# Performance work log

Hardware: AMD Instinct MI355X
Metric: run time of the kernel (lower is better)

The kernel has to match this reference:

```python
import jax, jax.numpy as jnp
import numpy as np

N_NODES = 50000
N_EDGES = 25000  # hyperedges
NNZ = 400000     # incidence pairs


def _segment_mean(x, idx, num_segments):
    s = jax.ops.segment_sum(x, idx, num_segments=num_segments)
    cnt = jax.ops.segment_sum(jnp.ones((x.shape[0], 1), x.dtype), idx, num_segments=num_segments)
    return s / jnp.maximum(cnt, 1.0)


def _unigcn_conv(X, W, vertex, edges, degE, degV):
    # X: [N, Cin] -> [N, Cout]
    X = X @ W                                   # linear (no bias)
    Xve = X[vertex]                             # gather per incidence [nnz, C]
    Xe = _segment_mean(Xve, edges, N_EDGES)     # first_aggregate='mean' over hyperedges
    Xe = Xe * degE                              # [M,1] scale
    Xev = Xe[edges]                             # gather back [nnz, C]
    Xv = jax.ops.segment_sum(Xev, vertex, num_segments=N_NODES)
    return Xv * degV                            # [N,1] scale


def setup_inputs() -> dict:
    key = jax.random.key(0)
    ks = jax.random.split(key, 8)
    nfeat, nhid_total, nclass = 512, 512, 40
    def glorot(k, fan_in, fan_out):
        std = np.sqrt(6.0 / (fan_in + fan_out))
        return jax.random.uniform(k, (fan_in, fan_out), jnp.float32, -std, std)
    return {
        "X": jax.random.normal(ks[0], (N_NODES, nfeat), jnp.float32),
        "vertex": jax.random.randint(ks[1], (NNZ,), 0, N_NODES, jnp.int32),
        "edges": jax.random.randint(ks[2], (NNZ,), 0, N_EDGES, jnp.int32),
        "W1": glorot(ks[3], nfeat, nhid_total),
        "W2": glorot(ks[4], nhid_total, nhid_total),
        "Wout": glorot(ks[5], nhid_total, nclass),
        "degE": jax.random.uniform(ks[6], (N_EDGES, 1), jnp.float32, 0.1, 1.0),
        "degV": jax.random.uniform(ks[7], (N_NODES, 1), jnp.float32, 0.1, 1.0),
    }


def reference(X, vertex, edges, W1, W2, Wout, degE, degV):
    # dropout layers are identity at eval (rates = 0)
    X = jax.nn.relu(_unigcn_conv(X, W1, vertex, edges, degE, degV))
    X = jax.nn.relu(_unigcn_conv(X, W2, vertex, edges, degE, degV))
    X = _unigcn_conv(X, Wout, vertex, edges, degE, degV)
    return jax.nn.log_softmax(X, axis=1)
```

## Files before the change

kernel.cpp:

```cpp
#include <hip/hip_runtime.h>

#define N_NODES 50000
#define N_EDGES_C 25000
#define NNZ_C 400000
#define SCHUNK 2048

typedef __bf16 bf16;
typedef __bf16 bf16x8 __attribute__((ext_vector_type(8)));
typedef __bf16 bf16x4 __attribute__((ext_vector_type(4)));
typedef float f32x4 __attribute__((ext_vector_type(4)));

typedef __attribute__((address_space(1))) const void as1_cvoid;
typedef __attribute__((address_space(3))) void as3_void;

__device__ __forceinline__ void gload_lds16(const bf16* g, bf16* l) {
  __builtin_amdgcn_global_load_lds((as1_cvoid*)g, (as3_void*)l, 16, 0, 0);
}

__global__ void hist_kernel(const int* __restrict__ vtx, const int* __restrict__ edg,
                            int* __restrict__ cntV, int* __restrict__ cntE, int nnz) {
  int i = blockIdx.x * blockDim.x + threadIdx.x;
  if (i < nnz) {
    atomicAdd(&cntV[vtx[i]], 1);
    atomicAdd(&cntE[edg[i]], 1);
  }
}

__global__ void scan_part2(const int* __restrict__ cntE, const int* __restrict__ cntV,
                           int* __restrict__ partE, int* __restrict__ partV,
                           int nbE) {
  __shared__ int red[256];
  const int t = threadIdx.x;
  const int isV = (blockIdx.x >= nbE);
  const int b = isV ? (blockIdx.x - nbE) : blockIdx.x;
  const int* cnt = isV ? cntV : cntE;
  const int n = isV ? N_NODES : N_EDGES_C;
  const int base = b * SCHUNK + t * 8;
  int s = 0;
#pragma unroll
  for (int q = 0; q < 8; ++q) {
    int i = base + q;
    if (i < n) s += cnt[i];
  }
  red[t] = s;
  __syncthreads();
  for (int d = 128; d > 0; d >>= 1) {
    if (t < d) red[t] += red[t + d];
    __syncthreads();
  }
  if (t == 0) (isV ? partV : partE)[b] = red[0];
}

__global__ void scan_mid2(int* __restrict__ partE, int* __restrict__ partV,
                          int* __restrict__ eoff, int* __restrict__ voff,
                          int nbE, int nbV) {
  const int wv = threadIdx.x >> 6;
  const int lane = threadIdx.x & 63;
  int* part = wv ? partV : partE;
  int* off = wv ? voff : eoff;
  const int np = wv ? nbV : nbE;
  const int n = wv ? N_NODES : N_EDGES_C;
  int orig = (lane < np) ? part[lane] : 0;
  int v = orig;
  for (int o = 1; o < 64; o <<= 1) {
    int x = __shfl_up(v, o);
    if (lane >= o) v += x;
  }
  if (lane < np) part[lane] = v - orig;
  if (lane == 63) off[n] = v;
}

__global__ void scan_final2(const int* __restrict__ cntE, const int* __restrict__ cntV,
                            const int* __restrict__ partE, const int* __restrict__ partV,
                            int* __restrict__ eoff, int* __restrict__ voff, int nbE) {
  __shared__ int tsum[256];
  const int t = threadIdx.x;
  const int isV = (blockIdx.x >= nbE);
  const int b = isV ? (blockIdx.x - nbE) : blockIdx.x;
  const int* cnt = isV ? cntV : cntE;
  const int* part = isV ? partV : partE;
  int* off = isV ? voff : eoff;
  const int n = isV ? N_NODES : N_EDGES_C;
  const int base = b * SCHUNK + t * 8;
  int loc[8];
  int s = 0;
#pragma unroll
  for (int q = 0; q < 8; ++q) {
    int i = base + q;
    loc[q] = (i < n) ? cnt[i] : 0;
    s += loc[q];
  }
  tsum[t] = s;
  __syncthreads();
  for (int d = 1; d < 256; d <<= 1) {
    int x = (t >= d) ? tsum[t - d] : 0;
    __syncthreads();
    tsum[t] += x;
    __syncthreads();
  }
  int run = part[b] + ((t > 0) ? tsum[t - 1] : 0);
#pragma unroll
  for (int q = 0; q < 8; ++q) {
    int i = base + q;
    if (i < n) off[i] = run;
    run += loc[q];
  }
}

__global__ void scatter_kernel(const int* __restrict__ vtx, const int* __restrict__ edg,
                               const int* __restrict__ eoff, const int* __restrict__ voff,
                               int* __restrict__ curE, int* __restrict__ curV,
                               int* __restrict__ evtx, int* __restrict__ vedg, int nnz) {
  int i = blockIdx.x * blockDim.x + threadIdx.x;
  if (i < nnz) {
    int e = edg[i], v = vtx[i];
    int p = atomicAdd(&curE[e], 1);
    evtx[eoff[e] + p] = v;
    int q = atomicAdd(&curV[v], 1);
    vedg[voff[v] + q] = e;
  }
}

__global__ void prep_conv(const float* __restrict__ W1, const float* __restrict__ W2,
                          const float* __restrict__ Wout, const float* __restrict__ X,
                          bf16* __restrict__ Wt1, bf16* __restrict__ Wt2,
                          bf16* __restrict__ Wt3, bf16* __restrict__ Xb) {
  const int b = blockIdx.x;
  const int t = threadIdx.x;
  if (b < 1024) {
    int idx = b * 256 + t;
    int n = idx >> 9, k = idx & 511;
    Wt1[idx] = (bf16)W1[(size_t)k * 512 + n];
  } else if (b < 2048) {
    int idx = (b - 1024) * 256 + t;
    int n = idx >> 9, k = idx & 511;
    Wt2[idx] = (bf16)W2[(size_t)k * 512 + n];
  } else if (b < 2304) {
    int idx = (b - 2048) * 256 + t;
    int n = idx >> 9, k = idx & 511;
    Wt3[idx] = (n < 40) ? (bf16)Wout[(size_t)k * 40 + n] : (bf16)0.0f;
  } else {
    size_t i = ((size_t)(b - 2304) * 256 + t) * 8;
    float4 v0 = *(const float4*)(X + i);
    float4 v1 = *(const float4*)(X + i + 4);
    bf16x8 o;
    o[0] = (bf16)v0.x; o[1] = (bf16)v0.y; o[2] = (bf16)v0.z; o[3] = (bf16)v0.w;
    o[4] = (bf16)v1.x; o[5] = (bf16)v1.y; o[6] = (bf16)v1.z; o[7] = (bf16)v1.w;
    *(bf16x8*)(Xb + i) = o;
  }
}

template <int TN>
__global__ __launch_bounds__(256) void gemm_bf16_kernel(
    const bf16* __restrict__ A, const bf16* __restrict__ B,
    bf16* __restrict__ Cb, int M, int K, int ldC, int Nstore) {
  __shared__ bf16 Al[2][128][64];
  __shared__ bf16 Bl[2][TN][64];
  const int bid = blockIdx.x;
  const int cpx = gridDim.x >> 3;
  const int wid = (bid & 7) * cpx + (bid >> 3);
  const int MBLK = (M + 127) >> 7;
  int mIdx, nIdx;
  if (TN == 128) { mIdx = wid >> 2; nIdx = wid & 3; }
  else           { mIdx = wid;      nIdx = 0; }
  if (mIdx >= MBLK) return;
  const int m0 = mIdx * 128;
  const int n0 = nIdx * TN;

  const int t = threadIdx.x;
  const int w = t >> 6, lane = t & 63;
  const int rb = (TN == 128) ? ((w >> 1) * 64) : (w * 32);
  const int cb = (TN == 128) ? ((w & 1) * 64) : 0;
  const int MF = (TN == 128) ? 4 : 2;
  const int lr = lane & 15;
  const int ls = lane >> 4;

  f32x4 acc[(TN == 128) ? 4 : 2][4];
#pragma unroll
  for (int m = 0; m < MF; ++m)
#pragma unroll
    for (int n = 0; n < 4; ++n) acc[m][n] = (f32x4){0.f, 0.f, 0.f, 0.f};

  const int srow8 = lane >> 3;
  const int scol = ((lane & 7) ^ srow8) << 3;

  const bf16* Abase = A + (size_t)m0 * K;
  const bf16* Bbase = B + (size_t)n0 * K;

#define STAGE(tile, bsel)                                                          \
  {                                                                                \
    const int kk_ = (tile) * 64;                                                   \
    _Pragma("unroll")                                                              \
    for (int q = 0; q < 4; ++q) {                                                  \
      const int row = w * 32 + q * 8 + srow8;                                      \
      gload_lds16(Abase + (size_t)row * K + kk_ + scol, &Al[bsel][w*32+q*8][0]);   \
    }                                                                              \
    _Pragma("unroll")                                                              \
    for (int q = 0; q < TN / 32; ++q) {                                            \
      const int row = w * (TN / 4) + q * 8 + srow8;                                \
      gload_lds16(Bbase + (size_t)row * K + kk_ + scol,                            \
                  &Bl[bsel][w * (TN / 4) + q * 8][0]);                             \
    }                                                                              \
  }

  const int NT = K >> 6;
  STAGE(0, 0);
  for (int tt = 0; tt < NT; ++tt) {
    const int cur = tt & 1;
    if (tt + 1 < NT) {
      STAGE(tt + 1, cur ^ 1);
      if (TN == 128) asm volatile("s_waitcnt vmcnt(8)" ::: "memory");
      else           asm volatile("s_waitcnt vmcnt(6)" ::: "memory");
    } else {
      asm volatile("s_waitcnt vmcnt(0)" ::: "memory");
    }
    __builtin_amdgcn_s_barrier();
    __builtin_amdgcn_s_setprio(1);
#pragma unroll
    for (int ks = 0; ks < 2; ++ks) {
      bf16x8 af[(TN == 128) ? 4 : 2], bfr[4];
#pragma unroll
      for (int m = 0; m < MF; ++m) {
        const int R = rb + m * 16 + lr;
        af[m] = *(const bf16x8*)(&Al[cur][R][((ks * 4 + ls) ^ (lr & 7)) << 3]);
      }
#pragma unroll
      for (int n = 0; n < 4; ++n) {
        const int R = cb + n * 16 + lr;
        bfr[n] = *(const bf16x8*)(&Bl[cur][R][((ks * 4 + ls) ^ (lr & 7)) << 3]);
      }
#pragma unroll
      for (int m = 0; m < MF; ++m)
#pragma unroll
        for (int n = 0; n < 4; ++n)
          acc[m][n] = __builtin_amdgcn_mfma_f32_16x16x32_bf16(af[m], bfr[n], acc[m][n], 0, 0, 0);
    }
    __builtin_amdgcn_s_setprio(0);
    __builtin_amdgcn_s_barrier();
  }
#undef STAGE

  const int cr = (lane >> 4) << 2;
  const int cc = lane & 15;
#pragma unroll
  for (int m = 0; m < MF; ++m) {
#pragma unroll
    for (int n = 0; n < 4; ++n) {
      int gc = n0 + cb + n * 16 + cc;
      if (gc >= Nstore) continue;
#pragma unroll
      for (int i = 0; i < 4; ++i) {
        int gr = m0 + rb + m * 16 + cr + i;
        if (gr < M) Cb[(size_t)gr * ldC + gc] = (bf16)acc[m][n][i];
      }
    }
  }
}

__global__ __launch_bounds__(256) void edge_agg_w(
    const bf16* __restrict__ Y, const int* __restrict__ eoff, const int* __restrict__ evtx,
    const float* __restrict__ degE, bf16* __restrict__ Xe, int nE) {
  const int wv = (blockIdx.x * 256 + threadIdx.x) >> 6;
  if (wv >= nE) return;
  const int lane = threadIdx.x & 63;
  const int beg = eoff[wv], end = eoff[wv + 1];
  const int cnt = end - beg;
  const float scale = (cnt > 0) ? degE[wv] / (float)cnt : 0.f;
  float acc[8] = {0.f, 0.f, 0.f, 0.f, 0.f, 0.f, 0.f, 0.f};
  for (int base = beg; base < end; base += 64) {
    const int nb = min(64, end - base);
    int myidx = (lane < nb) ? evtx[base + lane] : 0;
    int j = 0;
    for (; j + 1 < nb; j += 2) {
      const int i0 = __shfl(myidx, j);
      const int i1 = __shfl(myidx, j + 1);
      bf16x8 v0 = *(const bf16x8*)(Y + (size_t)i0 * 512 + lane * 8);
      bf16x8 v1 = *(const bf16x8*)(Y + (size_t)i1 * 512 + lane * 8);
#pragma unroll
      for (int q = 0; q < 8; ++q) acc[q] += (float)v0[q] + (float)v1[q];
    }
    if (j < nb) {
      const int i0 = __shfl(myidx, j);
      bf16x8 v0 = *(const bf16x8*)(Y + (size_t)i0 * 512 + lane * 8);
#pragma unroll
      for (int q = 0; q < 8; ++q) acc[q] += (float)v0[q];
    }
  }
  bf16x8 o;
#pragma unroll
  for (int q = 0; q < 8; ++q) o[q] = (bf16)(acc[q] * scale);
  *(bf16x8*)(Xe + (size_t)wv * 512 + lane * 8) = o;
}

__global__ __launch_bounds__(256) void vtx_agg_w(
    const bf16* __restrict__ Xe, const int* __restrict__ voff, const int* __restrict__ vedg,
    const float* __restrict__ degV, bf16* __restrict__ outB, int nV) {
  const int wv = (blockIdx.x * 256 + threadIdx.x) >> 6;
  if (wv >= nV) return;
  const int lane = threadIdx.x & 63;
  const int beg = voff[wv], end = voff[wv + 1];
  const float dv = degV[wv];
  float acc[8] = {0.f, 0.f, 0.f, 0.f, 0.f, 0.f, 0.f, 0.f};
  for (int base = beg; base < end; base += 64) {
    const int nb = min(64, end - base);
    int myidx = (lane < nb) ? vedg[base + lane] : 0;
    int j = 0;
    for (; j + 1 < nb; j += 2) {
      const int i0 = __shfl(myidx, j);
      const int i1 = __shfl(myidx, j + 1);
      bf16x8 v0 = *(const bf16x8*)(Xe + (size_t)i0 * 512 + lane * 8);
      bf16x8 v1 = *(const bf16x8*)(Xe + (size_t)i1 * 512 + lane * 8);
#pragma unroll
      for (int q = 0; q < 8; ++q) acc[q] += (float)v0[q] + (float)v1[q];
    }
    if (j < nb) {
      const int i0 = __shfl(myidx, j);
      bf16x8 v0 = *(const bf16x8*)(Xe + (size_t)i0 * 512 + lane * 8);
#pragma unroll
      for (int q = 0; q < 8; ++q) acc[q] += (float)v0[q];
    }
  }
  bf16x8 o;
#pragma unroll
  for (int q = 0; q < 8; ++q) o[q] = (bf16)fmaxf(acc[q] * dv, 0.f);
  *(bf16x8*)(outB + (size_t)wv * 512 + lane * 8) = o;
}

__global__ __launch_bounds__(256) void edge_agg40_w(
    const bf16* __restrict__ Y, const int* __restrict__ eoff, const int* __restrict__ evtx,
    const float* __restrict__ degE, bf16* __restrict__ Xe, int nE) {
  const int wv = (blockIdx.x * 256 + threadIdx.x) >> 6;
  if (wv >= nE) return;
  const int lane = threadIdx.x & 63;
  const int beg = eoff[wv], end = eoff[wv + 1];
  const int cnt = end - beg;
  const float scale = (cnt > 0) ? degE[wv] / (float)cnt : 0.f;
  float a0 = 0.f;
  for (int base = beg; base < end; base += 64) {
    const int nb = min(64, end - base);
    int myidx = (lane < nb) ? evtx[base + lane] : 0;
    int j = 0;
    for (; j + 3 < nb; j += 4) {
      const int i0 = __shfl(myidx, j);
      const int i1 = __shfl(myidx, j + 1);
      const int i2 = __shfl(myidx, j + 2);
      const int i3 = __shfl(myidx, j + 3);
      if (lane < 40) {
        float x0 = (float)Y[(size_t)i0 * 40 + lane];
        float x1 = (float)Y[(size_t)i1 * 40 + lane];
        float x2 = (float)Y[(size_t)i2 * 40 + lane];
        float x3 = (float)Y[(size_t)i3 * 40 + lane];
        a0 += (x0 + x1) + (x2 + x3);
      }
    }
    for (; j < nb; ++j) {
      const int i0 = __shfl(myidx, j);
      if (lane < 40) a0 += (float)Y[(size_t)i0 * 40 + lane];
    }
  }
  if (lane < 40) Xe[(size_t)wv * 40 + lane] = (bf16)(a0 * scale);
}

__global__ __launch_bounds__(256) void vtx_agg_lsm(
    const bf16* __restrict__ Xe, const int* __restrict__ voff, const int* __restrict__ vedg,
    const float* __restrict__ degV, float* __restrict__ out, int nV) {
  const int wv = (blockIdx.x * 256 + threadIdx.x) >> 6;
  if (wv >= nV) return;
  const int lane = threadIdx.x & 63;
  const int beg = voff[wv], end = voff[wv + 1];
  const float dv = degV[wv];
  float a0 = 0.f;
  for (int base = beg; base < end; base += 64) {
    const int nb = min(64, end - base);
    int myidx = (lane < nb) ? vedg[base + lane] : 0;
    int j = 0;
    for (; j + 3 < nb; j += 4) {
      const int i0 = __shfl(myidx, j);
      const int i1 = __shfl(myidx, j + 1);
      const int i2 = __shfl(myidx, j + 2);
      const int i3 = __shfl(myidx, j + 3);
      if (lane < 40) {
        float x0 = (float)Xe[(size_t)i0 * 40 + lane];
        float x1 = (float)Xe[(size_t)i1 * 40 + lane];
        float x2 = (float)Xe[(size_t)i2 * 40 + lane];
        float x3 = (float)Xe[(size_t)i3 * 40 + lane];
        a0 += (x0 + x1) + (x2 + x3);
      }
    }
    for (; j < nb; ++j) {
      const int i0 = __shfl(myidx, j);
      if (lane < 40) a0 += (float)Xe[(size_t)i0 * 40 + lane];
    }
  }
  a0 *= dv;
  float val = (lane < 40) ? a0 : -3.4e38f;
  float m = val;
#pragma unroll
  for (int o = 32; o > 0; o >>= 1) m = fmaxf(m, __shfl_xor(m, o));
  float ex = (lane < 40) ? expf(val - m) : 0.f;
  float s = ex;
#pragma unroll
  for (int o = 32; o > 0; o >>= 1) s += __shfl_xor(s, o);
  float ls = logf(s);
  if (lane < 40) out[(size_t)wv * 40 + lane] = val - m - ls;
}

extern "C" void kernel_launch(void* const* d_in, const int* in_sizes, int n_in,
                              void* d_out, int out_size, void* d_ws, size_t ws_size,
                              hipStream_t stream) {
  (void)in_sizes; (void)n_in; (void)out_size; (void)ws_size;
  const float* X = (const float*)d_in[0];
  const int* vertex = (const int*)d_in[1];
  const int* edges = (const int*)d_in[2];
  const float* W1 = (const float*)d_in[3];
  const float* W2 = (const float*)d_in[4];
  const float* Wout = (const float*)d_in[5];
  const float* degE = (const float*)d_in[6];
  const float* degV = (const float*)d_in[7];
  float* out = (float*)d_out;

  char* ws = (char*)d_ws;
  size_t off = 0;
  auto alloc = [&](size_t bytes) -> void* {
    void* p = ws + off;
    off += (bytes + 255) & ~(size_t)255;
    return p;
  };
  bf16* Xb  = (bf16*)alloc((size_t)N_NODES * 512 * sizeof(bf16));
  bf16* Yb  = (bf16*)alloc((size_t)N_NODES * 512 * sizeof(bf16));
  bf16* XeB = (bf16*)alloc((size_t)N_EDGES_C * 512 * sizeof(bf16));
  bf16* Y40b  = (bf16*)alloc((size_t)N_NODES * 40 * sizeof(bf16));
  bf16* Xe40b = (bf16*)alloc((size_t)N_EDGES_C * 40 * sizeof(bf16));
  bf16* Wt1 = (bf16*)alloc((size_t)512 * 512 * sizeof(bf16));
  bf16* Wt2 = (bf16*)alloc((size_t)512 * 512 * sizeof(bf16));
  bf16* Wt3 = (bf16*)alloc((size_t)128 * 512 * sizeof(bf16));
  int* eoff = (int*)alloc((N_EDGES_C + 1) * sizeof(int));
  int* voff = (int*)alloc((N_NODES + 1) * sizeof(int));
  int* evtx = (int*)alloc((size_t)NNZ_C * sizeof(int));
  int* vedg = (int*)alloc((size_t)NNZ_C * sizeof(int));
  int* cnts = (int*)alloc((size_t)(2 * (N_EDGES_C + N_NODES)) * sizeof(int));
  int* cntE = cnts;
  int* cntV = cnts + N_EDGES_C;
  int* curE = cnts + N_EDGES_C + N_NODES;
  int* curV = cnts + 2 * N_EDGES_C + N_NODES;
  int* partE = (int*)alloc(64 * sizeof(int));
  int* partV = (int*)alloc(64 * sizeof(int));

  hipMemsetAsync(cnts, 0, (size_t)(2 * (N_EDGES_C + N_NODES)) * sizeof(int), stream);

  prep_conv<<<2304 + 12500, 256, 0, stream>>>(W1, W2, Wout, X, Wt1, Wt2, Wt3, Xb);

  hist_kernel<<<(NNZ_C + 255) / 256, 256, 0, stream>>>(vertex, edges, cntV, cntE, NNZ_C);

  const int nbE = (N_EDGES_C + SCHUNK - 1) / SCHUNK;
  const int nbV = (N_NODES + SCHUNK - 1) / SCHUNK;
  scan_part2<<<nbE + nbV, 256, 0, stream>>>(cntE, cntV, partE, partV, nbE);
  scan_mid2<<<1, 128, 0, stream>>>(partE, partV, eoff, voff, nbE, nbV);
  scan_final2<<<nbE + nbV, 256, 0, stream>>>(cntE, cntV, partE, partV, eoff, voff, nbE);

  scatter_kernel<<<(NNZ_C + 255) / 256, 256, 0, stream>>>(vertex, edges, eoff, voff,
                                                          curE, curV, evtx, vedg, NNZ_C);

  const int MB = (N_NODES + 127) / 128;
  const int G512 = ((MB * 4 + 7) / 8) * 8;
  const int G64  = ((MB + 7) / 8) * 8;

  gemm_bf16_kernel<128><<<G512, 256, 0, stream>>>(Xb, Wt1, Yb, N_NODES, 512, 512, 512);
  edge_agg_w<<<(N_EDGES_C + 3) / 4, 256, 0, stream>>>(Yb, eoff, evtx, degE, XeB, N_EDGES_C);
  vtx_agg_w<<<(N_NODES + 3) / 4, 256, 0, stream>>>(XeB, voff, vedg, degV, Xb, N_NODES);

  gemm_bf16_kernel<128><<<G512, 256, 0, stream>>>(Xb, Wt2, Yb, N_NODES, 512, 512, 512);
  edge_agg_w<<<(N_EDGES_C + 3) / 4, 256, 0, stream>>>(Yb, eoff, evtx, degE, XeB, N_EDGES_C);
  vtx_agg_w<<<(N_NODES + 3) / 4, 256, 0, stream>>>(XeB, voff, vedg, degV, Xb, N_NODES);

  gemm_bf16_kernel<64><<<G64, 256, 0, stream>>>(Xb, Wt3, Y40b, N_NODES, 512, 40, 40);
  edge_agg40_w<<<(N_EDGES_C + 3) / 4, 256, 0, stream>>>(Y40b, eoff, evtx, degE, Xe40b, N_EDGES_C);
  vtx_agg_lsm<<<(N_NODES + 3) / 4, 256, 0, stream>>>(Xe40b, voff, vedg, degV, out, N_NODES);
}
```

Before: 498.8 us.

## Pad final-layer features to 64 and gather 16-byte vectors; fuse histogram into prep

The last layer's intermediate arrays are padded from 40 to 64 columns. The edge and vertex aggregation kernels now have 8 lane groups each load a bf16x8 vector per neighbour row, then reduce across groups with shuffles, replacing scalar per-lane loads. The log-softmax is rewritten over 8-wide chunks, and only the first 40 columns are written as vectors. Separately, the degree histogram is merged into the prep kernel's grid to save one launch. The padding adds bandwidth for the unused columns and relies on the GEMM writing zeros there.

```diff
diff --git a/kernel.cpp b/kernel.cpp
--- a/kernel.cpp
+++ b/kernel.cpp
@@ -9,6 +9,7 @@
 typedef __bf16 bf16x8 __attribute__((ext_vector_type(8)));
 typedef __bf16 bf16x4 __attribute__((ext_vector_type(4)));
 typedef float f32x4 __attribute__((ext_vector_type(4)));
+typedef float f32x8 __attribute__((ext_vector_type(8)));
 
 typedef __attribute__((address_space(1))) const void as1_cvoid;
 typedef __attribute__((address_space(3))) void as3_void;
@@ -17,12 +18,43 @@
   __builtin_amdgcn_global_load_lds((as1_cvoid*)g, (as3_void*)l, 16, 0, 0);
 }
 
-__global__ void hist_kernel(const int* __restrict__ vtx, const int* __restrict__ edg,
-                            int* __restrict__ cntV, int* __restrict__ cntE, int nnz) {
-  int i = blockIdx.x * blockDim.x + threadIdx.x;
-  if (i < nnz) {
-    atomicAdd(&cntV[vtx[i]], 1);
-    atomicAdd(&cntE[edg[i]], 1);
+#define PREP_W 2304
+#define PREP_X 12500
+#define PREP_H ((NNZ_C + 255) / 256)
+__global__ void prep_conv(const float* __restrict__ W1, const float* __restrict__ W2,
+                          const float* __restrict__ Wout, const float* __restrict__ X,
+                          bf16* __restrict__ Wt1, bf16* __restrict__ Wt2,
+                          bf16* __restrict__ Wt3,  bf16* __restrict__ Xb,
+                          const int* __restrict__ vtx, const int* __restrict__ edg,
+                          int* __restrict__ cntV, int* __restrict__ cntE) {
+  const int b = blockIdx.x;
+  const int t = threadIdx.x;
+  if (b < 1024) {
+    int idx = b * 256 + t;
+    int n = idx >> 9, k = idx & 511;
+    Wt1[idx] = (bf16)W1[(size_t)k * 512 + n];
+  } else if (b < 2048) {
+    int idx = (b - 1024) * 256 + t;
+    int n = idx >> 9, k = idx & 511;
+    Wt2[idx] = (bf16)W2[(size_t)k * 512 + n];
+  } else if (b < PREP_W) {
+    int idx = (b - 2048) * 256 + t;
+    int n = idx >> 9, k = idx & 511;
+    Wt3[idx] = (n < 40) ? (bf16)Wout[(size_t)k * 40 + n] : (bf16)0.0f;
+  } else if (b < PREP_W + PREP_X) {
+    size_t i = ((size_t)(b - PREP_W) * 256 + t) * 8;
+    float4 v0 = *(const float4*)(X + i);
+    float4 v1 = *(const float4*)(X + i + 4);
+    bf16x8 o;
+    o[0] = (bf16)v0.x; o[1] = (bf16)v0.y; o[2] = (bf16)v0.z; o[3] = (bf16)v0.w;
+    o[4] = (bf16)v1.x; o[5] = (bf16)v1.y; o[6] = (bf16)v1.z; o[7] = (bf16)v1.w;
+    *(bf16x8*)(Xb + i) = o;
+  } else {
+    int i = (b - PREP_W - PREP_X) * 256 + t;
+    if (i < NNZ_C) {
+      atomicAdd(&cntV[vtx[i]], 1);
+      atomicAdd(&cntE[edg[i]], 1);
+    }
   }
 }
 
@@ -118,35 +150,6 @@
     evtx[eoff[e] + p] = v;
     int q = atomicAdd(&curV[v], 1);
     vedg[voff[v] + q] = e;
-  }
-}
-
-__global__ void prep_conv(const float* __restrict__ W1, const float* __restrict__ W2,
-                          const float* __restrict__ Wout, const float* __restrict__ X,
-                          bf16* __restrict__ Wt1, bf16* __restrict__ Wt2,
-                          bf16* __restrict__ Wt3, bf16* __restrict__ Xb) {
-  const int b = blockIdx.x;
-  const int t = threadIdx.x;
-  if (b < 1024) {
-    int idx = b * 256 + t;
-    int n = idx >> 9, k = idx & 511;
-    Wt1[idx] = (bf16)W1[(size_t)k * 512 + n];
-  } else if (b < 2048) {
-    int idx = (b - 1024) * 256 + t;
-    int n = idx >> 9, k = idx & 511;
-    Wt2[idx] = (bf16)W2[(size_t)k * 512 + n];
-  } else if (b < 2304) {
-    int idx = (b - 2048) * 256 + t;
-    int n = idx >> 9, k = idx & 511;
-    Wt3[idx] = (n < 40) ? (bf16)Wout[(size_t)k * 40 + n] : (bf16)0.0f;
-  } else {
-    size_t i = ((size_t)(b - 2304) * 256 + t) * 8;
-    float4 v0 = *(const float4*)(X + i);
-    float4 v1 = *(const float4*)(X + i + 4);
-    bf16x8 o;
-    o[0] = (bf16)v0.x; o[1] = (bf16)v0.y; o[2] = (bf16)v0.z; o[3] = (bf16)v0.w;
-    o[4] = (bf16)v1.x; o[5] = (bf16)v1.y; o[6] = (bf16)v1.z; o[7] = (bf16)v1.w;
-    *(bf16x8*)(Xb + i) = o;
   }
 }
 
@@ -326,83 +329,95 @@
   *(bf16x8*)(outB + (size_t)wv * 512 + lane * 8) = o;
 }
 
-__global__ __launch_bounds__(256) void edge_agg40_w(
+__global__ __launch_bounds__(256) void edge_agg40_w8(
     const bf16* __restrict__ Y, const int* __restrict__ eoff, const int* __restrict__ evtx,
     const float* __restrict__ degE, bf16* __restrict__ Xe, int nE) {
   const int wv = (blockIdx.x * 256 + threadIdx.x) >> 6;
   if (wv >= nE) return;
   const int lane = threadIdx.x & 63;
+  const int g = lane >> 3, c = lane & 7;
   const int beg = eoff[wv], end = eoff[wv + 1];
   const int cnt = end - beg;
   const float scale = (cnt > 0) ? degE[wv] / (float)cnt : 0.f;
-  float a0 = 0.f;
+  float acc[8] = {0.f, 0.f, 0.f, 0.f, 0.f, 0.f, 0.f, 0.f};
   for (int base = beg; base < end; base += 64) {
     const int nb = min(64, end - base);
     int myidx = (lane < nb) ? evtx[base + lane] : 0;
-    int j = 0;
-    for (; j + 3 < nb; j += 4) {
-      const int i0 = __shfl(myidx, j);
-      const int i1 = __shfl(myidx, j + 1);
-      const int i2 = __shfl(myidx, j + 2);
-      const int i3 = __shfl(myidx, j + 3);
-      if (lane < 40) {
-        float x0 = (float)Y[(size_t)i0 * 40 + lane];
-        float x1 = (float)Y[(size_t)i1 * 40 + lane];
-        float x2 = (float)Y[(size_t)i2 * 40 + lane];
-        float x3 = (float)Y[(size_t)i3 * 40 + lane];
-        a0 += (x0 + x1) + (x2 + x3);
+    for (int inner = 0; inner < 8; ++inner) {
+      const int r = inner * 8 + g;
+      if (inner * 8 >= nb) break;
+      const int ridx = __shfl(myidx, r);
+      if (r < nb) {
+        bf16x8 v = *(const bf16x8*)(Y + (size_t)ridx * 64 + c * 8);
+#pragma unroll
+        for (int q = 0; q < 8; ++q) acc[q] += (float)v[q];
       }
     }
-    for (; j < nb; ++j) {
-      const int i0 = __shfl(myidx, j);
-      if (lane < 40) a0 += (float)Y[(size_t)i0 * 40 + lane];
-    }
-  }
-  if (lane < 40) Xe[(size_t)wv * 40 + lane] = (bf16)(a0 * scale);
-}
-
-__global__ __launch_bounds__(256) void vtx_agg_lsm(
+  }
+#pragma unroll
+  for (int o = 8; o < 64; o <<= 1)
+#pragma unroll
+    for (int q = 0; q < 8; ++q) acc[q] += __shfl_xor(acc[q], o);
+  if (lane < 8) {
+    bf16x8 o;
+#pragma unroll
+    for (int q = 0; q < 8; ++q) o[q] = (bf16)(acc[q] * scale);
+    *(bf16x8*)(Xe + (size_t)wv * 64 + lane * 8) = o;
+  }
+}
+
+__global__ __launch_bounds__(256) void vtx_agg_lsm8(
     const bf16* __restrict__ Xe, const int* __restrict__ voff, const int* __restrict__ vedg,
     const float* __restrict__ degV, float* __restrict__ out, int nV) {
   const int wv = (blockIdx.x * 256 + threadIdx.x) >> 6;
   if (wv >= nV) return;
   const int lane = threadIdx.x & 63;
+  const int g = lane >> 3, c = lane & 7;
   const int beg = voff[wv], end = voff[wv + 1];
   const float dv = degV[wv];
-  float a0 = 0.f;
+  float acc[8] = {0.f, 0.f, 0.f, 0.f, 0.f, 0.f, 0.f, 0.f};
   for (int base = beg; base < end; base += 64) {
     const int nb = min(64, end - base);
     int myidx = (lane < nb) ? vedg[base + lane] : 0;
-    int j = 0;
-    for (; j + 3 < nb; j += 4) {
-      const int i0 = __shfl(myidx, j);
-      const int i1 = __shfl(myidx, j + 1);
-      const int i2 = __shfl(myidx, j + 2);
-      const int i3 = __shfl(myidx, j + 3);
-      if (lane < 40) {
-        float x0 = (float)Xe[(size_t)i0 * 40 + lane];
-        float x1 = (float)Xe[(size_t)i1 * 40 + lane];
-        float x2 = (float)Xe[(size_t)i2 * 40 + lane];
-        float x3 = (float)Xe[(size_t)i3 * 40 + lane];
-        a0 += (x0 + x1) + (x2 + x3);
+    for (int inner = 0; inner < 8; ++inner) {
+      const int r = inner * 8 + g;
+      if (inner * 8 >= nb) break;
+      const int ridx = __shfl(myidx, r);
+      if (r < nb) {
+        bf16x8 v = *(const bf16x8*)(Xe + (size_t)ridx * 64 + c * 8);
+#pragma unroll
+        for (int q = 0; q < 8; ++q) acc[q] += (float)v[q];
       }
     }
-    for (; j < nb; ++j) {
-      const int i0 = __shfl(myidx, j);
-      if (lane < 40) a0 += (float)Xe[(size_t)i0 * 40 + lane];
-    }
-  }
-  a0 *= dv;
-  float val = (lane < 40) ? a0 : -3.4e38f;
-  float m = val;
-#pragma unroll
-  for (int o = 32; o > 0; o >>= 1) m = fmaxf(m, __shfl_xor(m, o));
-  float ex = (lane < 40) ? expf(val - m) : 0.f;
-  float s = ex;
-#pragma unroll
-  for (int o = 32; o > 0; o >>= 1) s += __shfl_xor(s, o);
-  float ls = logf(s);
-  if (lane < 40) out[(size_t)wv * 40 + lane] = val - m - ls;
+  }
+#pragma unroll
+  for (int o = 8; o < 64; o <<= 1)
+#pragma unroll
+    for (int q = 0; q < 8; ++q) acc[q] += __shfl_xor(acc[q], o);
+  float l[8];
+#pragma unroll
+  for (int q = 0; q < 8; ++q) l[q] = acc[q] * dv;
+  float lm = -3.4e38f;
+  if (c < 5) {
+#pragma unroll
+    for (int q = 0; q < 8; ++q) lm = fmaxf(lm, l[q]);
+  }
+#pragma unroll
+  for (int o = 1; o < 8; o <<= 1) lm = fmaxf(lm, __shfl_xor(lm, o));
+  float ls = 0.f;
+  if (c < 5) {
+#pragma unroll
+    for (int q = 0; q < 8; ++q) ls += expf(l[q] - lm);
+  }
+#pragma unroll
+  for (int o = 1; o < 8; o <<= 1) ls += __shfl_xor(ls, o);
+  const float lg = logf(ls);
+  if (lane < 5) {
+    f32x8 w;
+#pragma unroll
+    for (int q = 0; q < 8; ++q) w[q] = l[q] - lm - lg;
+    *(f32x8*)(out + (size_t)wv * 40 + lane * 8) = w;
+  }
 }
 
 extern "C" void kernel_launch(void* const* d_in, const int* in_sizes, int n_in,
@@ -429,8 +444,8 @@
   bf16* Xb  = (bf16*)alloc((size_t)N_NODES * 512 * sizeof(bf16));
   bf16* Yb  = (bf16*)alloc((size_t)N_NODES * 512 * sizeof(bf16));
   bf16* XeB = (bf16*)alloc((size_t)N_EDGES_C * 512 * sizeof(bf16));
-  bf16* Y40b  = (bf16*)alloc((size_t)N_NODES * 40 * sizeof(bf16));
-  bf16* Xe40b = (bf16*)alloc((size_t)N_EDGES_C * 40 * sizeof(bf16));
+  bf16* Y40b  = (bf16*)alloc((size_t)N_NODES * 64 * sizeof(bf16));
+  bf16* Xe40b = (bf16*)alloc((size_t)N_EDGES_C * 64 * sizeof(bf16));
   bf16* Wt1 = (bf16*)alloc((size_t)512 * 512 * sizeof(bf16));
   bf16* Wt2 = (bf16*)alloc((size_t)512 * 512 * sizeof(bf16));
   bf16* Wt3 = (bf16*)alloc((size_t)128 * 512 * sizeof(bf16));
@@ -448,9 +463,8 @@
 
   hipMemsetAsync(cnts, 0, (size_t)(2 * (N_EDGES_C + N_NODES)) * sizeof(int), stream);
 
-  prep_conv<<<2304 + 12500, 256, 0, stream>>>(W1, W2, Wout, X, Wt1, Wt2, Wt3, Xb);
-
-  hist_kernel<<<(NNZ_C + 255) / 256, 256, 0, stream>>>(vertex, edges, cntV, cntE, NNZ_C);
+  prep_conv<<<PREP_W + PREP_X + PREP_H, 256, 0, stream>>>(
+      W1, W2, Wout, X, Wt1, Wt2, Wt3, Xb, vertex, edges, cntV, cntE);
 
   const int nbE = (N_EDGES_C + SCHUNK - 1) / SCHUNK;
   const int nbV = (N_NODES + SCHUNK - 1) / SCHUNK;
@@ -473,7 +487,7 @@
   edge_agg_w<<<(N_EDGES_C + 3) / 4, 256, 0, stream>>>(Yb, eoff, evtx, degE, XeB, N_EDGES_C);
   vtx_agg_w<<<(N_NODES + 3) / 4, 256, 0, stream>>>(XeB, voff, vedg, degV, Xb, N_NODES);
 
-  gemm_bf16_kernel<64><<<G64, 256, 0, stream>>>(Xb, Wt3, Y40b, N_NODES, 512, 40, 40);
-  edge_agg40_w<<<(N_EDGES_C + 3) / 4, 256, 0, stream>>>(Y40b, eoff, evtx, degE, Xe40b, N_EDGES_C);
-  vtx_agg_lsm<<<(N_NODES + 3) / 4, 256, 0, stream>>>(Xe40b, voff, vedg, degV, out, N_NODES);
-}
+  gemm_bf16_kernel<64><<<G64, 256, 0, stream>>>(Xb, Wt3, Y40b, N_NODES, 512, 64, 64);
+  edge_agg40_w8<<<(N_EDGES_C + 3) / 4, 256, 0, stream>>>(Y40b, eoff, evtx, degE, Xe40b, N_EDGES_C);
+  vtx_agg_lsm8<<<(N_NODES + 3) / 4, 256, 0, stream>>>(Xe40b, voff, vedg, degV, out, N_NODES);
+}
```

Result: no change. 498.4 us (-0.1%).
